# Kernel optimization log

Measured on AMD Instinct MI355X. Metric: run time of the kernel, lower is better.

## Reference

```python
import jax, jax.numpy as jnp
import numpy as np

B = 4096       # batch
S = 4096       # seq_len == input_dim
DEPTH = 2
D_MODEL = 1
D_FFN = 2      # d_model * d_ffn_factor
EPS = 1e-5


def _layernorm(x, w, b):
    mu = jnp.mean(x, axis=-1, keepdims=True)
    var = jnp.mean((x - mu) ** 2, axis=-1, keepdims=True)
    return (x - mu) * jax.lax.rsqrt(var + EPS) * w + b


def setup_inputs() -> dict:
    key = jax.random.key(0)
    ks = jax.random.split(key, 16)
    sc = lambda fan_in: 1.0 / np.sqrt(fan_in)
    inp = {
        "x": jax.random.normal(ks[0], (B, S), dtype=jnp.float32),
        # per-depth stacked gMLP block params
        "ln1_w": jnp.ones((DEPTH, D_MODEL), jnp.float32),
        "ln1_b": jnp.zeros((DEPTH, D_MODEL), jnp.float32),
        "cp1_w": jax.random.uniform(ks[1], (DEPTH, D_FFN, D_MODEL), jnp.float32, -sc(D_MODEL), sc(D_MODEL)),
        "cp1_b": jax.random.uniform(ks[2], (DEPTH, D_FFN), jnp.float32, -sc(D_MODEL), sc(D_MODEL)),
        "sgu_ln_w": jnp.ones((DEPTH, D_FFN // 2), jnp.float32),
        "sgu_ln_b": jnp.zeros((DEPTH, D_FFN // 2), jnp.float32),
        "sgu_proj_w": jax.random.uniform(ks[3], (DEPTH, S, S), jnp.float32, -sc(S), sc(S)),
        "sgu_proj_b": jax.random.uniform(ks[4], (DEPTH, S), jnp.float32, -sc(S), sc(S)),
        "cp2_w": jax.random.uniform(ks[5], (DEPTH, D_MODEL, D_FFN // 2), jnp.float32, -sc(D_FFN // 2), sc(D_FFN // 2)),
        "cp2_b": jax.random.uniform(ks[6], (DEPTH, D_MODEL), jnp.float32, -sc(D_FFN // 2), sc(D_FFN // 2)),
        "pooler_w": jax.random.uniform(ks[7], (S, S), jnp.float32, -sc(S), sc(S)),
        "pooler_b": jax.random.uniform(ks[8], (S,), jnp.float32, -sc(S), sc(S)),
        "cls_w": jax.random.uniform(ks[9], (1, S), jnp.float32, -sc(S), sc(S)),
        "cls_b": jax.random.uniform(ks[10], (1,), jnp.float32, -sc(S), sc(S)),
    }
    return inp


def reference(x, ln1_w, ln1_b, cp1_w, cp1_b, sgu_ln_w, sgu_ln_b,
              sgu_proj_w, sgu_proj_b, cp2_w, cp2_b,
              pooler_w, pooler_b, cls_w, cls_b):
    gelu = lambda t: jax.nn.gelu(t, approximate=False)
    h = x[..., None]                                   # [B, S, 1]
    for i in range(DEPTH):
        res = h
        t = _layernorm(h, ln1_w[i], ln1_b[i])          # [B, S, 1]
        t = gelu(t @ cp1_w[i].T + cp1_b[i])            # [B, S, 2]
        u, v = t[..., :D_FFN // 2], t[..., D_FFN // 2:]
        v = _layernorm(v, sgu_ln_w[i], sgu_ln_b[i])
        # transpose(1,2) -> Linear(S,S) -> transpose back, fused as einsum
        v = jnp.einsum('st,btc->bsc', sgu_proj_w[i], v) + sgu_proj_b[i][:, None]
        h = u * v                                      # [B, S, 1]
        h = h @ cp2_w[i].T + cp2_b[i] + res            # [B, S, 1]
    out = h[..., 0]                                    # [B, S]
    out = gelu(out @ pooler_w.T + pooler_b)            # [B, S]
    logits = out @ cls_w.T + cls_b                     # [B, 1]
    return logits[..., 0]                              # [B]
```

## Files before the change

### kernel.cpp

```cpp
#include <hip/hip_runtime.h>


#define K_DIM 4096

typedef __bf16 bf16x8 __attribute__((ext_vector_type(8)));
typedef float f32x4 __attribute__((ext_vector_type(4)));

__device__ __forceinline__ ushort f2bf(float f) {
    unsigned int u = __float_as_uint(f);
    u = (u + 0x7fffu + ((u >> 16) & 1u)) >> 16;
    return (ushort)u;
}

__device__ __forceinline__ float gelu_exact(float x) {
    return 0.5f * x * (1.0f + erff(x * 0.70710678118654752440f));
}

__device__ __forceinline__ void gld16(const void* g, void* l) {
    __builtin_amdgcn_global_load_lds(
        (__attribute__((address_space(1))) void*)(g),
        (__attribute__((address_space(3))) void*)(l), 16, 0, 0);
}

__global__ __launch_bounds__(256) void c_kernel(const float* __restrict__ ln1_b,
                                                const float* __restrict__ cp1_w,
                                                const float* __restrict__ cp1_b,
                                                const float* __restrict__ sgu_ln_b,
                                                const float* __restrict__ sgu_proj_w,
                                                const float* __restrict__ sgu_proj_b,
                                                const float* __restrict__ cp2_w,
                                                const float* __restrict__ cp2_b,
                                                const float* __restrict__ cls_b,
                                                const float* __restrict__ pooler_b,
                                                float* __restrict__ c,
                                                float* __restrict__ e,
                                                float* __restrict__ out) {
    int t = blockIdx.x * 256 + threadIdx.x;
    float cv = 0.0f;
#pragma unroll
    for (int i = 0; i < 2; ++i) {
        float alpha = gelu_exact(ln1_b[i] * cp1_w[i * 2 + 0] + cp1_b[i * 2 + 0]);
        float beta  = sgu_ln_b[i];
        float Ri = 0.0f;
        if (beta != 0.0f) {
            const float* pr = sgu_proj_w + ((size_t)i * 4096 + t) * K_DIM;
            for (int k = 0; k < K_DIM; k += 4) {
                float4 pv = *(const float4*)&pr[k];
                Ri += pv.x + pv.y + pv.z + pv.w;
            }
        }
        float v = beta * Ri + sgu_proj_b[i * 4096 + t];
        cv += alpha * v * cp2_w[i] + cp2_b[i];
    }
    c[t]   = cv;
    e[t]   = pooler_b[t];
    out[t] = cls_b[0];
}

__global__ __launch_bounds__(256) void cvt2_kernel(const float* __restrict__ s0,
                                                   ushort* __restrict__ d0,
                                                   const float* __restrict__ s1,
                                                   ushort* __restrict__ d1,
                                                   const float* __restrict__ c,
                                                   float* __restrict__ e) {
    int b = blockIdx.x;
    bool isP = (b >= 8192);
    const float* src = isP ? s1 : s0;
    ushort* dst = isP ? d1 : d0;
    int i = (b & 8191) * 256 + threadIdx.x;
    const float4* s4 = (const float4*)src + (size_t)i * 2;
    float4 a = s4[0], q = s4[1];
    union { ushort u[8]; uint4 v; } r;
    r.u[0] = f2bf(a.x); r.u[1] = f2bf(a.y); r.u[2] = f2bf(a.z); r.u[3] = f2bf(a.w);
    r.u[4] = f2bf(q.x); r.u[5] = f2bf(q.y); r.u[6] = f2bf(q.z); r.u[7] = f2bf(q.w);
    ((uint4*)dst)[i] = r.v;
    if (isP) {
        int col = (i << 3) & 4095;
        float s = a.x * c[col + 0] + a.y * c[col + 1] + a.z * c[col + 2] + a.w * c[col + 3]
                + q.x * c[col + 4] + q.y * c[col + 5] + q.z * c[col + 6] + q.w * c[col + 7];
#pragma unroll
        for (int m = 1; m < 64; m <<= 1) s += __shfl_xor(s, m);
        if ((threadIdx.x & 63) == 0) atomicAdd(&e[i >> 9], s);
    }
}

__global__ __launch_bounds__(512, 2) void gemm_kernel(const ushort* __restrict__ X,
                                                      const ushort* __restrict__ P,
                                                      const float* __restrict__ clsW,
                                                      const float* __restrict__ e,
                                                      float* __restrict__ accOut) {
    __shared__ __align__(16) ushort As[2][256 * 64];
    __shared__ __align__(16) ushort Bs[2][256 * 64];

    const int t = threadIdx.x;
    const int flat = blockIdx.x;
    const int swz = (flat & 7) * 32 + (flat >> 3);
    const int bRow = swz >> 4, bCol = swz & 15;

    const int lane = t & 63, wv = t >> 6;
    const int g = lane >> 4, lo = lane & 15;
    const int wm = wv >> 2, wn = wv & 3;

    f32x4 zero4 = {0.f, 0.f, 0.f, 0.f};
    f32x4 acc[8][4];
#pragma unroll
    for (int mi = 0; mi < 8; ++mi)
#pragma unroll
        for (int ni = 0; ni < 4; ++ni) acc[mi][ni] = zero4;

    const int sr = t >> 3;
    const int cs = (t & 7) ^ (sr & 7);
    const ushort* gA = X + (size_t)(bRow * 256 + sr) * K_DIM + cs * 8;
    const ushort* gB = P + (size_t)(bCol * 256 + sr) * K_DIM + cs * 8;
    char* lA0 = (char*)&As[0][0] + t * 16;
    char* lB0 = (char*)&Bs[0][0] + t * 16;

#define STAGE(buf, k0)                                                            \
    do {                                                                          \
        _Pragma("unroll") for (int r_ = 0; r_ < 4; ++r_)                          \
            gld16(gA + (size_t)(r_ * 64) * K_DIM + (k0), lA0 + (buf)*32768 + r_ * 8192); \
        _Pragma("unroll") for (int r_ = 0; r_ < 4; ++r_)                          \
            gld16(gB + (size_t)(r_ * 64) * K_DIM + (k0), lB0 + (buf)*32768 + r_ * 8192); \
    } while (0)

#define COMPUTE(buf)                                                              \
    do {                                                                          \
        _Pragma("unroll") for (int kk = 0; kk < 2; ++kk) {                        \
            const int ch = (((kk << 2) | g) ^ (lo & 7)) << 3;                     \
            bf16x8 af[8], bfr[4];                                                 \
            _Pragma("unroll") for (int mi = 0; mi < 8; ++mi)                      \
                af[mi] = *(const bf16x8*)&As[buf][(wm * 128 + mi * 16 + lo) * 64 + ch]; \
            _Pragma("unroll") for (int ni = 0; ni < 4; ++ni)                      \
                bfr[ni] = *(const bf16x8*)&Bs[buf][(wn * 64 + ni * 16 + lo) * 64 + ch]; \
            __builtin_amdgcn_s_setprio(1);                                        \
            _Pragma("unroll") for (int mi = 0; mi < 8; ++mi)                      \
                _Pragma("unroll") for (int ni = 0; ni < 4; ++ni)                  \
                    acc[mi][ni] = __builtin_amdgcn_mfma_f32_16x16x32_bf16(        \
                        af[mi], bfr[ni], acc[mi][ni], 0, 0, 0);                   \
            __builtin_amdgcn_s_setprio(0);                                        \
        }                                                                         \
    } while (0)

    STAGE(0, 0);
#pragma unroll 1
    for (int k0 = 64; k0 < 3968; k0 += 128) {
        STAGE(1, k0);
        asm volatile("s_waitcnt vmcnt(8)\n\ts_barrier" ::: "memory");
        COMPUTE(0);
        asm volatile("s_barrier" ::: "memory");
        STAGE(0, k0 + 64);
        asm volatile("s_waitcnt vmcnt(8)\n\ts_barrier" ::: "memory");
        COMPUTE(1);
        asm volatile("s_barrier" ::: "memory");
    }
    STAGE(1, 4032);
    asm volatile("s_waitcnt vmcnt(8)\n\ts_barrier" ::: "memory");
    COMPUTE(0);
    asm volatile("s_barrier" ::: "memory");
    asm volatile("s_waitcnt vmcnt(0)\n\ts_barrier" ::: "memory");
    COMPUTE(1);

#undef STAGE
#undef COMPUTE

    int sColBase = bCol * 256 + wn * 64 + lo;
    float eb[4], cw[4];
#pragma unroll
    for (int ni = 0; ni < 4; ++ni) {
        int s = sColBase + ni * 16;
        eb[ni] = e[s];
        cw[ni] = clsW[s];
    }
#pragma unroll
    for (int mi = 0; mi < 8; ++mi) {
        int rowBase = bRow * 256 + wm * 128 + mi * 16 + g * 4;
#pragma unroll
        for (int r = 0; r < 4; ++r) {
            float sum = 0.0f;
#pragma unroll
            for (int ni = 0; ni < 4; ++ni) {
                float y = acc[mi][ni][r] + eb[ni];
                sum += gelu_exact(y) * cw[ni];
            }
            sum += __shfl_xor(sum, 1);
            sum += __shfl_xor(sum, 2);
            sum += __shfl_xor(sum, 4);
            sum += __shfl_xor(sum, 8);
            if (lo == 0) atomicAdd(&accOut[rowBase + r], sum);
        }
    }
}

extern "C" void kernel_launch(void* const* d_in, const int* in_sizes, int n_in,
                              void* d_out, int out_size, void* d_ws, size_t ws_size,
                              hipStream_t stream) {
    const float* x          = (const float*)d_in[0];
    const float* ln1_b      = (const float*)d_in[2];
    const float* cp1_w      = (const float*)d_in[3];
    const float* cp1_b      = (const float*)d_in[4];
    const float* sgu_ln_b   = (const float*)d_in[6];
    const float* sgu_proj_w = (const float*)d_in[7];
    const float* sgu_proj_b = (const float*)d_in[8];
    const float* cp2_w      = (const float*)d_in[9];
    const float* cp2_b      = (const float*)d_in[10];
    const float* pooler_w   = (const float*)d_in[11];
    const float* pooler_b   = (const float*)d_in[12];
    const float* cls_w      = (const float*)d_in[13];
    const float* cls_b      = (const float*)d_in[14];

    ushort* xb = (ushort*)d_ws;
    ushort* pb = xb + (size_t)K_DIM * K_DIM;
    float*  fs = (float*)(pb + (size_t)K_DIM * K_DIM);
    float* c_buf = fs;
    float* e_buf = fs + 4096;
    float* out   = (float*)d_out;

    c_kernel<<<16, 256, 0, stream>>>(ln1_b, cp1_w, cp1_b, sgu_ln_b, sgu_proj_w,
                                     sgu_proj_b, cp2_w, cp2_b, cls_b, pooler_b,
                                     c_buf, e_buf, out);
    cvt2_kernel<<<16384, 256, 0, stream>>>(x, xb, pooler_w, pb, c_buf, e_buf);
    gemm_kernel<<<256, 512, 0, stream>>>(xb, pb, cls_w, e_buf, out);
}
```

Before: 410.0 us.

## Split GEMM mainloop into eight-phase quadrant schedule with interleaved staging

Restructures the pooler GEMM main loop into eight phases per 128-wide K step. Each phase computes one quadrant of the per-wave tile and issues half-tile global-to-LDS loads for later stages alongside it. The warp-to-tile mapping changes to interleaved quadrants, and the epilogue indexing is updated to match. The aim is a finer overlap of LDS reads, global prefetch and MFMA issue, similar to the hipBLASLt/HipKittens 8-wave ping-pong style, at the cost of many more barriers per iteration.

```diff
diff --git a/kernel.cpp b/kernel.cpp
--- a/kernel.cpp
+++ b/kernel.cpp
@@ -108,72 +108,93 @@
 #pragma unroll
         for (int ni = 0; ni < 4; ++ni) acc[mi][ni] = zero4;
 
-    const int sr = t >> 3;
-    const int cs = (t & 7) ^ (sr & 7);
-    const ushort* gA = X + (size_t)(bRow * 256 + sr) * K_DIM + cs * 8;
-    const ushort* gB = P + (size_t)(bCol * 256 + sr) * K_DIM + cs * 8;
+    const int sr2 = t >> 3;
+    const int cs = (t & 7) ^ (sr2 & 7);
+    const ushort* gA = X + (size_t)(bRow * 256 + sr2) * K_DIM + cs * 8;
+    const ushort* gB = P + (size_t)(bCol * 256 + sr2) * K_DIM + cs * 8;
     char* lA0 = (char*)&As[0][0] + t * 16;
     char* lB0 = (char*)&Bs[0][0] + t * 16;
 
-#define STAGE(buf, k0)                                                            \
-    do {                                                                          \
-        _Pragma("unroll") for (int r_ = 0; r_ < 4; ++r_)                          \
-            gld16(gA + (size_t)(r_ * 64) * K_DIM + (k0), lA0 + (buf)*32768 + r_ * 8192); \
-        _Pragma("unroll") for (int r_ = 0; r_ < 4; ++r_)                          \
-            gld16(gB + (size_t)(r_ * 64) * K_DIM + (k0), lB0 + (buf)*32768 + r_ * 8192); \
+#define STAGE_A(buf, h, k0)                                                        \
+    do {                                                                           \
+        gld16(gA + (size_t)((h) * 128) * K_DIM + (k0), lA0 + (buf) * 32768 + (h) * 16384);      \
+        gld16(gA + (size_t)((h) * 128 + 64) * K_DIM + (k0), lA0 + (buf) * 32768 + (h) * 16384 + 8192); \
     } while (0)
-
-#define COMPUTE(buf)                                                              \
-    do {                                                                          \
-        _Pragma("unroll") for (int kk = 0; kk < 2; ++kk) {                        \
-            const int ch = (((kk << 2) | g) ^ (lo & 7)) << 3;                     \
-            bf16x8 af[8], bfr[4];                                                 \
-            _Pragma("unroll") for (int mi = 0; mi < 8; ++mi)                      \
-                af[mi] = *(const bf16x8*)&As[buf][(wm * 128 + mi * 16 + lo) * 64 + ch]; \
-            _Pragma("unroll") for (int ni = 0; ni < 4; ++ni)                      \
-                bfr[ni] = *(const bf16x8*)&Bs[buf][(wn * 64 + ni * 16 + lo) * 64 + ch]; \
-            __builtin_amdgcn_s_setprio(1);                                        \
-            _Pragma("unroll") for (int mi = 0; mi < 8; ++mi)                      \
-                _Pragma("unroll") for (int ni = 0; ni < 4; ++ni)                  \
-                    acc[mi][ni] = __builtin_amdgcn_mfma_f32_16x16x32_bf16(        \
-                        af[mi], bfr[ni], acc[mi][ni], 0, 0, 0);                   \
-            __builtin_amdgcn_s_setprio(0);                                        \
-        }                                                                         \
+#define STAGE_B(buf, h, k0)                                                        \
+    do {                                                                           \
+        gld16(gB + (size_t)((h) * 128) * K_DIM + (k0), lB0 + (buf) * 32768 + (h) * 16384);      \
+        gld16(gB + (size_t)((h) * 128 + 64) * K_DIM + (k0), lB0 + (buf) * 32768 + (h) * 16384 + 8192); \
     } while (0)
 
-    STAGE(0, 0);
+#define VMW4 asm volatile("s_waitcnt vmcnt(4)" ::: "memory")
+#define VMW0 asm volatile("s_waitcnt vmcnt(0)" ::: "memory")
+#define NOSTAGE ((void)0)
+#define NOWAIT ((void)0)
+
+#define PHASE(buf, qm, qn, STG, WAIT)                                              \
+    do {                                                                           \
+        bf16x8 af[4][2], bfr[2][2];                                                \
+        _Pragma("unroll") for (int m_ = 0; m_ < 4; ++m_)                           \
+            _Pragma("unroll") for (int kk_ = 0; kk_ < 2; ++kk_)                    \
+                af[m_][kk_] = *(const bf16x8*)&As[buf][((qm) * 128 + wm * 64 + m_ * 16 + lo) * 64 + ((((kk_ << 2) | g) ^ (lo & 7)) << 3)]; \
+        _Pragma("unroll") for (int n_ = 0; n_ < 2; ++n_)                           \
+            _Pragma("unroll") for (int kk_ = 0; kk_ < 2; ++kk_)                    \
+                bfr[n_][kk_] = *(const bf16x8*)&Bs[buf][((qn) * 128 + wn * 32 + n_ * 16 + lo) * 64 + ((((kk_ << 2) | g) ^ (lo & 7)) << 3)]; \
+        STG;                                                                       \
+        __builtin_amdgcn_s_barrier();                                              \
+        asm volatile("s_waitcnt lgkmcnt(0)" ::: "memory");                         \
+        __builtin_amdgcn_sched_barrier(0);                                         \
+        __builtin_amdgcn_s_setprio(1);                                             \
+        _Pragma("unroll") for (int m_ = 0; m_ < 4; ++m_)                           \
+            _Pragma("unroll") for (int n_ = 0; n_ < 2; ++n_)                       \
+                _Pragma("unroll") for (int kk_ = 0; kk_ < 2; ++kk_)                \
+                    acc[(qm) * 4 + m_][(qn) * 2 + n_] = __builtin_amdgcn_mfma_f32_16x16x32_bf16( \
+                        af[m_][kk_], bfr[n_][kk_], acc[(qm) * 4 + m_][(qn) * 2 + n_], 0, 0, 0); \
+        __builtin_amdgcn_s_setprio(0);                                             \
+        WAIT;                                                                      \
+        __builtin_amdgcn_s_barrier();                                              \
+    } while (0)
+
+    STAGE_A(0, 0, 0);  STAGE_B(0, 0, 0);
+    STAGE_A(0, 1, 0);  STAGE_B(0, 1, 0);
+    STAGE_A(1, 0, 64); STAGE_B(1, 0, 64);
+    VMW4;
+    __builtin_amdgcn_s_barrier();
+
 #pragma unroll 1
-    for (int k0 = 64; k0 < 3968; k0 += 128) {
-        STAGE(1, k0);
-        asm volatile("s_waitcnt vmcnt(8)\n\ts_barrier" ::: "memory");
-        COMPUTE(0);
-        asm volatile("s_barrier" ::: "memory");
-        STAGE(0, k0 + 64);
-        asm volatile("s_waitcnt vmcnt(8)\n\ts_barrier" ::: "memory");
-        COMPUTE(1);
-        asm volatile("s_barrier" ::: "memory");
-    }
-    STAGE(1, 4032);
-    asm volatile("s_waitcnt vmcnt(8)\n\ts_barrier" ::: "memory");
-    COMPUTE(0);
-    asm volatile("s_barrier" ::: "memory");
-    asm volatile("s_waitcnt vmcnt(0)\n\ts_barrier" ::: "memory");
-    COMPUTE(1);
-
-#undef STAGE
-#undef COMPUTE
-
-    int sColBase = bCol * 256 + wn * 64 + lo;
+    for (int k0 = 0; k0 < 3968; k0 += 128) {
+        PHASE(0, 0, 0, STAGE_A(1, 1, k0 + 64),  NOWAIT);
+        PHASE(0, 0, 1, STAGE_B(1, 1, k0 + 64),  NOWAIT);
+        PHASE(0, 1, 0, STAGE_A(0, 0, k0 + 128), NOWAIT);
+        PHASE(0, 1, 1, STAGE_B(0, 0, k0 + 128), VMW4);
+        PHASE(1, 0, 0, STAGE_A(0, 1, k0 + 128), NOWAIT);
+        PHASE(1, 0, 1, STAGE_B(0, 1, k0 + 128), NOWAIT);
+        PHASE(1, 1, 0, STAGE_A(1, 0, k0 + 192), NOWAIT);
+        PHASE(1, 1, 1, STAGE_B(1, 0, k0 + 192), VMW4);
+    }
+    PHASE(0, 0, 0, STAGE_A(1, 1, 4032), NOWAIT);
+    PHASE(0, 0, 1, STAGE_B(1, 1, 4032), NOWAIT);
+    PHASE(0, 1, 0, NOSTAGE, NOWAIT);
+    PHASE(0, 1, 1, NOSTAGE, VMW0);
+    PHASE(1, 0, 0, NOSTAGE, NOWAIT);
+    PHASE(1, 0, 1, NOSTAGE, NOWAIT);
+    PHASE(1, 1, 0, NOSTAGE, NOWAIT);
+    PHASE(1, 1, 1, NOSTAGE, NOWAIT);
+
+#undef PHASE
+#undef STAGE_A
+#undef STAGE_B
+
     float eb[4], cw[4];
 #pragma unroll
     for (int ni = 0; ni < 4; ++ni) {
-        int s = sColBase + ni * 16;
+        int s = bCol * 256 + (ni >> 1) * 128 + wn * 32 + (ni & 1) * 16 + lo;
         eb[ni] = e[s];
         cw[ni] = clsW[s];
     }
 #pragma unroll
     for (int mi = 0; mi < 8; ++mi) {
-        int rowBase = bRow * 256 + wm * 128 + mi * 16 + g * 4;
+        int rowBase = bRow * 256 + (mi >> 2) * 128 + wm * 64 + (mi & 3) * 16 + g * 4;
 #pragma unroll
         for (int r = 0; r < 4; ++r) {
             float sum = 0.0f;
```

Measured after the change: 429.8 us. 1.05x slower.
